# Performance work log

Measured on AMD Instinct MI355X. Metric: run time of the kernel, lower is better.

## Reference

```python
import jax, jax.numpy as jnp
import numpy as np

D_MODEL, D_STATE, D_CONV, EXPAND, N_HEADS = 768, 64, 4, 2, 12
D_INNER = D_MODEL * EXPAND           # 1536
HEAD_DIM = D_INNER // N_HEADS        # 128
IN_PROJ = D_INNER * 2 + N_HEADS * D_STATE * 2 + N_HEADS  # 4620
EPS = 1e-5


def setup_inputs() -> dict:
    key = jax.random.key(0)
    ks = jax.random.split(key, 8)
    s = lambda fan_in: 1.0 / np.sqrt(fan_in)
    return {
        "x": jax.random.normal(ks[0], (1, 1024, D_MODEL), dtype=jnp.float32),
        "W_in": jax.random.normal(ks[1], (IN_PROJ, D_MODEL), dtype=jnp.float32) * s(D_MODEL),
        "conv_w": jax.random.normal(ks[2], (D_INNER, D_CONV), dtype=jnp.float32) * s(D_CONV),
        "conv_b": jnp.zeros((D_INNER,), dtype=jnp.float32),
        "A_log": jnp.full((N_HEADS,), np.log(0.5), dtype=jnp.float32),
        "Dp": jnp.ones((N_HEADS,), dtype=jnp.float32),
        "dt_bias": jnp.zeros((N_HEADS,), dtype=jnp.float32),
        "W_out": jax.random.normal(ks[3], (D_MODEL, D_INNER), dtype=jnp.float32) * s(D_INNER),
        "norm_w": jnp.ones((D_INNER,), dtype=jnp.float32),
    }


def _causal_conv1d(x, w, b):
    # x: (B,L,Din), depthwise causal conv with kernel size D_CONV
    L = x.shape[1]
    xp = jnp.pad(x, ((0, 0), (D_CONV - 1, 0), (0, 0)))
    y = b
    for i in range(D_CONV):  # fixed small kernel, unrolled
        y = y + xp[:, i:i + L, :] * w[:, i]
    return y


def reference(x, W_in, conv_w, conv_b, A_log, Dp, dt_bias, W_out, norm_w):
    B_sz, L, _ = x.shape
    nh, ds, hd = N_HEADS, D_STATE, HEAD_DIM
    proj = jnp.einsum('bld,pd->blp', x, W_in)
    z = proj[:, :, :D_INNER]
    x_ssm = proj[:, :, D_INNER:2 * D_INNER]
    o = 2 * D_INNER
    Bm = proj[:, :, o:o + nh * ds].reshape(B_sz, L, nh, ds)
    Cm = proj[:, :, o + nh * ds:o + 2 * nh * ds].reshape(B_sz, L, nh, ds)
    dt_r = proj[:, :, o + 2 * nh * ds:]
    dt = jax.nn.softplus(dt_r) + dt_bias[None, None, :]          # (B,L,nh)

    x_ssm = jax.nn.silu(_causal_conv1d(x_ssm, conv_w, conv_b))
    x_ssm = x_ssm.reshape(B_sz, L, nh, hd)

    A = -jnp.exp(A_log)                                          # (nh,)
    log_decay = A[None, None, :] * dt                            # (B,L,nh)
    Phi = jnp.cumsum(log_decay, axis=1)
    dB = dt[..., None] * Bm                                      # (B,L,nh,ds)
    # b: (B,L,nh,hd,ds) outer product
    b = dB[:, :, :, None, :] * x_ssm[..., None]
    max_exp = 80.0
    exp_neg_Phi = jnp.exp(jnp.minimum(-Phi, max_exp))[..., None, None]
    b_cumsum = jnp.cumsum(exp_neg_Phi * b, axis=1)
    h = jnp.exp(Phi)[..., None, None] * b_cumsum                 # (B,L,nh,hd,ds)
    y = jnp.sum(Cm[:, :, :, None, :] * h, axis=-1)               # (B,L,nh,hd)
    y = y + Dp[None, None, :, None] * x_ssm
    y = y.reshape(B_sz, L, D_INNER)

    # RMSNorm then gate
    rms = jax.lax.rsqrt(jnp.mean(y * y, axis=-1, keepdims=True) + EPS)
    y = y * rms * norm_w
    y = y * jax.nn.silu(z)
    return jnp.einsum('bli,di->bld', y, W_out)
```

## Files before the change

### kernel.cpp

```cpp
#include <hip/hip_runtime.h>
#include <cmath>

#define LSEQ   1024
#define NPROJ  4620
#define NPADW  4736
#define DINNER 1536
#define NH     12
#define HDIM   128
#define OFF_Z  0
#define OFF_X  1536
#define OFF_B  3072
#define OFF_C  3840
#define OFF_DT 4608

typedef unsigned short u16;
typedef unsigned int u32;
typedef short bf16x8 __attribute__((ext_vector_type(8)));
typedef float f32x4 __attribute__((ext_vector_type(4)));

__device__ inline u16 f2b(float f) {
  unsigned u = __float_as_uint(f);
  return (u16)((u + 0x7fffu + ((u >> 16) & 1u)) >> 16);
}
__device__ inline float b2f(u16 h) { return __uint_as_float(((unsigned)h) << 16); }
__device__ inline u32 pk2(float a, float b) { return (u32)f2b(a) | ((u32)f2b(b) << 16); }

__device__ inline void gll16(const void* g, void* l) {
  __builtin_amdgcn_global_load_lds((const __attribute__((address_space(1))) void*)g,
                                   (__attribute__((address_space(3))) void*)l, 16, 0, 0);
}

#define S0N 196608
#define S1N 909312
#define S1V 887040
#define S2N 294912
__global__ __launch_bounds__(256) void ksplit_all(const float* __restrict__ x,
    const float* __restrict__ Wi, u16* __restrict__ Ah, u16* __restrict__ Wh) {
  int i = blockIdx.x * 256 + threadIdx.x;
  const float* src; u16* hi; int j, valid;
  if (i < S0N) { src = x;  hi = Ah; j = i;       valid = S0N; }
  else         { src = Wi; hi = Wh; j = i - S0N; valid = S1V; }
  float4 v = (j < valid) ? ((const float4*)src)[j] : make_float4(0.f, 0.f, 0.f, 0.f);
  ((uint2*)hi)[j] = make_uint2(pk2(v.x, v.y), pk2(v.z, v.w));
}

template<int BM, int BN, int MAP, bool NG>
__global__ __launch_bounds__(256) void gemm1(const u16* __restrict__ Ah,
    const u16* __restrict__ Wh, float* __restrict__ C,
    int lda, int ldw, int Ksl, int Nreal, int ldc) {
  constexpr int PLA = BM * 64;
  constexpr int IA = BM / 8, ITOT = IA + BN / 8;
  constexpr int FRn = BN / 32;
  __shared__ u16 lds[PLA + BN * 64];
  const int tid = threadIdx.x;
  const int l = tid & 63, w = tid >> 6;
  const int wm = w >> 1, wn = w & 1;
  const int kg = l >> 4, li = l & 15;

  int b = blockIdx.x, m0, n0, koff;
  float* Cp = C;
  if (MAP == 0) {
    int xcd = b & 7, idx = b >> 3;
    m0 = (idx & 15) * 64;
    n0 = (xcd * 5 + (idx >> 4)) * 128;
    koff = 0;
    if (NG && n0 >= NPADW) return;
  } else {
    int xcd = b & 7, idx = b >> 3;
    int gg = xcd * 6 + (idx >> 4);
    m0 = (idx & 15) * 64;
    n0 = (gg % 12) * 64;
    koff = (gg / 12) * 384;
    Cp = C + (size_t)(gg / 12) * LSEQ * ldc;
  }

  const int srcg = ((l & 7) ^ (l >> 3)) * 8;
  auto stage = [&](int t) {
    const int k0 = koff + t * 64;
    for (int q = w; q < ITOT; q += 4) {
      const u16* gb; int r0b, ldk, dst;
      if (q < IA) { gb = Ah; r0b = m0 + 8 * q;        dst = 8 * q * 64;              ldk = lda; }
      else        { gb = Wh; r0b = n0 + 8 * (q - IA); dst = PLA + 8 * (q - IA) * 64; ldk = ldw; }
      gll16(gb + (size_t)(r0b + (l >> 3)) * ldk + k0 + srcg, &lds[dst]);
    }
  };
  auto rd = [&](int region, int row, int ks) -> bf16x8 {
    return *(const bf16x8*)&lds[region + row * 64 + (((ks * 4 + kg) ^ (row & 7)) << 3)];
  };

  f32x4 acc[2][FRn];
#pragma unroll
  for (int m = 0; m < 2; ++m)
#pragma unroll
    for (int n = 0; n < FRn; ++n) acc[m][n] = (f32x4){0.f, 0.f, 0.f, 0.f};

  const int NT = Ksl / 64;
  stage(0);
  asm volatile("s_waitcnt vmcnt(0)" ::: "memory");
  __syncthreads();
  for (int t = 0; t < NT; ++t) {
    bf16x8 af[2][2], wf[FRn][2];
#pragma unroll
    for (int ks = 0; ks < 2; ++ks) {
#pragma unroll
      for (int m = 0; m < 2; ++m)
        af[m][ks] = rd(0, wm * 32 + m * 16 + li, ks);
#pragma unroll
      for (int n = 0; n < FRn; ++n)
        wf[n][ks] = rd(PLA, wn * (BN / 2) + n * 16 + li, ks);
    }
    __syncthreads();
    if (t + 1 < NT) stage(t + 1);
#pragma unroll
    for (int ks = 0; ks < 2; ++ks)
#pragma unroll
      for (int m = 0; m < 2; ++m)
#pragma unroll
        for (int n = 0; n < FRn; ++n)
          acc[m][n] = __builtin_amdgcn_mfma_f32_16x16x32_bf16(af[m][ks], wf[n][ks], acc[m][n], 0, 0, 0);
    if (t + 1 < NT) {
      asm volatile("s_waitcnt vmcnt(0)" ::: "memory");
      __syncthreads();
    }
  }
#pragma unroll
  for (int m = 0; m < 2; ++m) {
    int rbase = m0 + wm * 32 + m * 16 + kg * 4;
#pragma unroll
    for (int n = 0; n < FRn; ++n) {
      int col = n0 + wn * (BN / 2) + n * 16 + li;
      if (!NG || col < Nreal) {
#pragma unroll
        for (int r = 0; r < 4; ++r)
          Cp[(size_t)(rbase + r) * ldc + col] = acc[m][n][r];
      }
    }
  }
}

__global__ __launch_bounds__(256) void addk(const float* __restrict__ P,
    const float* __restrict__ rmsacc, float* __restrict__ out) {
  const int S = LSEQ * 768 / 4;
  int i = blockIdx.x * 256 + threadIdx.x;
  int t = i / 192;
  float rms = rsqrtf(rmsacc[t] * (1.f / 1536.f) + 1e-5f);
  float4 a = ((const float4*)P)[i];
  float4 b = ((const float4*)P)[i + S];
  float4 c = ((const float4*)P)[i + 2 * S];
  float4 d = ((const float4*)P)[i + 3 * S];
  ((float4*)out)[i] = make_float4((a.x + b.x + c.x + d.x) * rms,
                                  (a.y + b.y + c.y + d.y) * rms,
                                  (a.z + b.z + c.z + d.z) * rms,
                                  (a.w + b.w + c.w + d.w) * rms);
}

__global__ __launch_bounds__(256) void conv_state(const float* __restrict__ proj,
    const float* __restrict__ cw, const float* __restrict__ cb,
    const float* __restrict__ A_log, const float* __restrict__ dt_bias,
    u16* __restrict__ xactT, float* __restrict__ SlocF,
    float* __restrict__ Phi, float* __restrict__ dts, float* __restrict__ rmsacc) {
  const int k = blockIdx.x, h = blockIdx.y, tid = threadIdx.x;
  const int l = tid & 63, w = tid >> 6, kg = l >> 4, li = l & 15;
  __shared__ u16 Bw[4096];
  __shared__ u16 Xt[8192];
  __shared__ float wS[64];
  __shared__ float wsum[4];
  __shared__ float phiC[64], dtC[64];
  const int s0 = k * 64;

  if (h == 0 && tid < 64) rmsacc[k * 64 + tid] = 0.f;
  {
    float Ac = -expf(A_log[h]);
    float bb = dt_bias[h];
    float v[4], s = 0.f;
#pragma unroll
    for (int u = 0; u < 4; ++u) {
      int t = tid * 4 + u;
      float xr = proj[(size_t)t * NPROJ + OFF_DT + h];
      float sp = (xr > 20.f) ? xr : log1pf(expf(xr));
      v[u] = sp + bb;
      s += v[u];
    }
    int lane = tid & 63, wv = tid >> 6;
    float ps = s;
#pragma unroll
    for (int d = 1; d < 64; d <<= 1) {
      float o = __shfl_up(ps, d);
      if (lane >= d) ps += o;
    }
    if (lane == 63) wsum[wv] = ps;
    __syncthreads();
    float off = 0.f;
    for (int q = 0; q < wv; ++q) off += wsum[q];
    float run = off + ps - s;
#pragma unroll
    for (int u = 0; u < 4; ++u) {
      int t = tid * 4 + u;
      run += v[u];
      if ((t >> 6) == k) {
        float ph = Ac * run;
        phiC[t & 63] = ph;
        dtC[t & 63] = v[u];
        Phi[t * NH + h] = ph;
        dts[t * NH + h] = v[u];
      }
    }
  }
  __syncthreads();
  if (tid < 64) wS[tid] = expf(phiC[63] + fminf(-phiC[tid], 80.f)) * dtC[tid];
  __syncthreads();
#pragma unroll
  for (int u = 0; u < 4; ++u) {
    int idx = tid + u * 256, s = idx >> 4, q = (idx & 15) * 4;
    float4 v = *(const float4*)(proj + (size_t)(s0 + s) * NPROJ + OFF_B + h * 64 + q);
    float ws_ = wS[s];
    float vv[4] = {v.x, v.y, v.z, v.w};
#pragma unroll
    for (int j = 0; j < 4; ++j) {
      int d = q + j;
      Bw[d * 64 + (((s >> 3) ^ (d & 7)) << 3) + (s & 7)] = f2b(vv[j] * ws_);
    }
  }
  {
    int c = tid & 127, th = tid >> 7;
    int cg = h * HDIM + c;
    float w0 = cw[cg * 4], w1 = cw[cg * 4 + 1], w2 = cw[cg * 4 + 2], w3 = cw[cg * 4 + 3];
    float bias = cb[cg];
    int tb = s0 + th * 32;
    auto P = [&](int t) { return (t >= 0) ? proj[(size_t)t * NPROJ + OFF_X + cg] : 0.f; };
    float x0 = P(tb - 3), x1 = P(tb - 2), x2 = P(tb - 1);
    u32 pkb[16];
    float prev = 0.f;
#pragma unroll
    for (int i = 0; i < 32; ++i) {
      float x3 = P(tb + i);
      float a = bias;
      a = fmaf(x0, w0, a); a = fmaf(x1, w1, a); a = fmaf(x2, w2, a); a = fmaf(x3, w3, a);
      float sv = a / (1.f + expf(-a));
      if (i & 1) pkb[i >> 1] = pk2(prev, sv); else prev = sv;
      x0 = x1; x1 = x2; x2 = x3;
    }
#pragma unroll
    for (int g = 0; g < 4; ++g) {
      int sg = th * 4 + g;
      *(uint4*)&Xt[c * 64 + ((sg ^ (c & 7)) << 3)] =
          make_uint4(pkb[g * 4], pkb[g * 4 + 1], pkb[g * 4 + 2], pkb[g * 4 + 3]);
    }
    size_t xo = ((size_t)(k * NH + h) * 128 + c) * 64 + th * 32;
#pragma unroll
    for (int g = 0; g < 4; ++g)
      *(uint4*)(xactT + xo + g * 8) =
          make_uint4(pkb[g * 4], pkb[g * 4 + 1], pkb[g * 4 + 2], pkb[g * 4 + 3]);
  }
  __syncthreads();
  const int wm = w >> 1, wn = w & 1;
  auto rd = [&](const u16* reg, int row, int ks) -> bf16x8 {
    return *(const bf16x8*)&reg[row * 64 + (((ks * 4 + kg) ^ (row & 7)) << 3)];
  };
  f32x4 acc[4][2];
#pragma unroll
  for (int m = 0; m < 4; ++m)
#pragma unroll
    for (int n = 0; n < 2; ++n) acc[m][n] = (f32x4){0.f, 0.f, 0.f, 0.f};
#pragma unroll
  for (int ks = 0; ks < 2; ++ks) {
    bf16x8 xf[4], bf[2];
#pragma unroll
    for (int m = 0; m < 4; ++m) xf[m] = rd(Xt, wm * 64 + m * 16 + li, ks);
#pragma unroll
    for (int n = 0; n < 2; ++n) bf[n] = rd(Bw, wn * 32 + n * 16 + li, ks);
#pragma unroll
    for (int m = 0; m < 4; ++m)
#pragma unroll
      for (int n = 0; n < 2; ++n)
        acc[m][n] = __builtin_amdgcn_mfma_f32_16x16x32_bf16(xf[m], bf[n], acc[m][n], 0, 0, 0);
  }
  float* dst = SlocF + (((size_t)(k * NH + h)) << 13);
#pragma unroll
  for (int m = 0; m < 4; ++m)
#pragma unroll
    for (int n = 0; n < 2; ++n)
#pragma unroll
      for (int r = 0; r < 4; ++r) {
        int c = wm * 64 + m * 16 + kg * 4 + r;
        int d = wn * 32 + n * 16 + li;
        dst[c * 64 + d] = acc[m][n][r];
      }
}

__global__ __launch_bounds__(256) void chunk_scan(const float* __restrict__ SlocF,
    u16* __restrict__ SlocT, const float* __restrict__ Phi,
    const float* __restrict__ Wo, u16* __restrict__ Woh) {
  int gi = blockIdx.x * 256 + threadIdx.x;
#pragma unroll
  for (int it = 0; it < 3; ++it) {
    int j = gi + it * 98304;
    float4 vv = ((const float4*)Wo)[j];
    ((uint2*)Woh)[j] = make_uint2(pk2(vv.x, vv.y), pk2(vv.z, vv.w));
  }
  int b = blockIdx.x;
  int h = b >> 5;
  int e = (b & 31) * 256 + threadIdx.x;
  float run = SlocF[((size_t)h << 13) + e];
  SlocT[((size_t)h << 13) + e] = f2b(run);
#pragma unroll
  for (int k = 1; k < 16; ++k) {
    float lam = expf(Phi[(k * 64 + 63) * NH + h] - Phi[(k * 64 - 1) * NH + h]);
    size_t o = ((size_t)(k * NH + h) << 13) + e;
    run = fmaf(lam, run, SlocF[o]);
    SlocT[o] = f2b(run);
  }
}

__global__ __launch_bounds__(256) void ssm_out(const float* __restrict__ proj,
    const u16* __restrict__ xactT, const float* __restrict__ Phi,
    const float* __restrict__ dts, const float* __restrict__ Dp,
    const u16* __restrict__ SlocT, const float* __restrict__ nw,
    u16* __restrict__ Yh, float* __restrict__ rmsacc) {
  const int k = blockIdx.x, h = blockIdx.y, zh = blockIdx.z, tid = threadIdx.x;
  const int l = tid & 63, w = tid >> 6, kg = l >> 4, li = l & 15;
  const int wm = w >> 1, wn = w & 1;
  __shared__ u16 Cs[4096], Bs[4096], Ps[4096], Xs[4096], Ss[4096];
  __shared__ float phiT[64], eSs[64], dSs[64], eTs[64];
  __shared__ float sq[64], nws[64];
  const int t0 = k * 64;
  const int srcg = ((l & 7) ^ (l >> 3)) * 8;
  {
#pragma unroll
    for (int j = 0; j < 2; ++j) {
      int rb = w * 16 + j * 8;
      gll16(xactT + ((size_t)(k * NH + h) * 128 + zh * 64 + rb + (l >> 3)) * 64 + srcg, &Xs[rb * 64]);
    }
    if (k > 0) {
      const u16* ssrc = SlocT + (((size_t)((k - 1) * NH + h) * 128 + zh * 64)) * 64;
#pragma unroll
      for (int j = 0; j < 2; ++j) {
        int rb = w * 16 + j * 8;
        gll16(ssrc + (size_t)(rb + (l >> 3)) * 64 + srcg, &Ss[rb * 64]);
      }
    }
  }
#pragma unroll
  for (int u = 0; u < 4; ++u) {
    int idx = tid + u * 256, i = idx >> 4, q = (idx & 15) * 4;
    int aoff = i * 64 + (((q >> 3) ^ (i & 7)) << 3) + (q & 4);
    float4 cv = *(const float4*)(proj + (size_t)(t0 + i) * NPROJ + OFF_C + h * 64 + q);
    float4 bv = *(const float4*)(proj + (size_t)(t0 + i) * NPROJ + OFF_B + h * 64 + q);
    *(uint2*)&Cs[aoff] = make_uint2(pk2(cv.x, cv.y), pk2(cv.z, cv.w));
    *(uint2*)&Bs[aoff] = make_uint2(pk2(bv.x, bv.y), pk2(bv.z, bv.w));
  }
  if (tid < 64) {
    float p = Phi[(t0 + tid) * NH + h];
    phiT[tid] = p;
    eSs[tid] = fminf(-p, 80.f);
    dSs[tid] = dts[(t0 + tid) * NH + h];
    eTs[tid] = (k > 0) ? expf(p - Phi[(t0 - 1) * NH + h]) : 0.f;
    sq[tid] = 0.f;
    nws[tid] = nw[h * HDIM + zh * 64 + tid];
  }
  __syncthreads();
  auto rd = [&](const u16* reg, int row, int ks) -> bf16x8 {
    return *(const bf16x8*)&reg[row * 64 + (((ks * 4 + kg) ^ (row & 7)) << 3)];
  };
  bf16x8 Cf[2][2];
  f32x4 accS[2][2];
#pragma unroll
  for (int m = 0; m < 2; ++m)
#pragma unroll
    for (int n = 0; n < 2; ++n) accS[m][n] = (f32x4){0.f, 0.f, 0.f, 0.f};
#pragma unroll
  for (int ks = 0; ks < 2; ++ks) {
    bf16x8 Bf[2];
#pragma unroll
    for (int m = 0; m < 2; ++m) Cf[m][ks] = rd(Cs, wm * 32 + m * 16 + li, ks);
#pragma unroll
    for (int n = 0; n < 2; ++n) Bf[n] = rd(Bs, wn * 32 + n * 16 + li, ks);
#pragma unroll
    for (int m = 0; m < 2; ++m)
#pragma unroll
      for (int n = 0; n < 2; ++n)
        accS[m][n] = __builtin_amdgcn_mfma_f32_16x16x32_bf16(Cf[m][ks], Bf[n], accS[m][n], 0, 0, 0);
  }
#pragma unroll
  for (int m = 0; m < 2; ++m)
#pragma unroll
    for (int n = 0; n < 2; ++n)
#pragma unroll
      for (int r = 0; r < 4; ++r) {
        int t = wm * 32 + m * 16 + kg * 4 + r;
        int s = wn * 32 + n * 16 + li;
        float f = (s <= t) ? expf(phiT[t] + eSs[s]) * dSs[s] : 0.f;
        Ps[t * 64 + (((s >> 3) ^ (t & 7)) << 3) + (s & 7)] = f2b(accS[m][n][r] * f);
      }
  __syncthreads();
  f32x4 accY[2][2], acc2[2][2];
#pragma unroll
  for (int m = 0; m < 2; ++m)
#pragma unroll
    for (int n = 0; n < 2; ++n) {
      accY[m][n] = (f32x4){0.f, 0.f, 0.f, 0.f};
      acc2[m][n] = (f32x4){0.f, 0.f, 0.f, 0.f};
    }
#pragma unroll
  for (int ks = 0; ks < 2; ++ks) {
    bf16x8 Pf[2], Xf[2];
#pragma unroll
    for (int m = 0; m < 2; ++m) Pf[m] = rd(Ps, wm * 32 + m * 16 + li, ks);
#pragma unroll
    for (int n = 0; n < 2; ++n) Xf[n] = rd(Xs, wn * 32 + n * 16 + li, ks);
#pragma unroll
    for (int m = 0; m < 2; ++m)
#pragma unroll
      for (int n = 0; n < 2; ++n)
        accY[m][n] = __builtin_amdgcn_mfma_f32_16x16x32_bf16(Pf[m], Xf[n], accY[m][n], 0, 0, 0);
    if (k > 0) {
      bf16x8 Sf[2];
#pragma unroll
      for (int n = 0; n < 2; ++n) Sf[n] = rd(Ss, wn * 32 + n * 16 + li, ks);
#pragma unroll
      for (int m = 0; m < 2; ++m)
#pragma unroll
        for (int n = 0; n < 2; ++n)
          acc2[m][n] = __builtin_amdgcn_mfma_f32_16x16x32_bf16(Cf[m][ks], Sf[n], acc2[m][n], 0, 0, 0);
    }
  }
  float dp = Dp[h];
  float ls[8] = {};
#pragma unroll
  for (int m = 0; m < 2; ++m)
#pragma unroll
    for (int n = 0; n < 2; ++n)
#pragma unroll
      for (int r = 0; r < 4; ++r) {
        int t = wm * 32 + m * 16 + kg * 4 + r;
        int c = wn * 32 + n * 16 + li;
        float xv = b2f(Xs[c * 64 + (((t >> 3) ^ (c & 7)) << 3) + (t & 7)]);
        float val = accY[m][n][r] + eTs[t] * acc2[m][n][r] + dp * xv;
        ls[m * 4 + r] = fmaf(val, val, ls[m * 4 + r]);
        float z = proj[(size_t)(t0 + t) * NPROJ + OFF_Z + h * HDIM + zh * 64 + c];
        float sz = z / (1.f + expf(-z));
        Yh[(size_t)(t0 + t) * DINNER + h * HDIM + zh * 64 + c] = f2b(val * nws[c] * sz);
      }
#pragma unroll
  for (int j = 0; j < 8; ++j) {
    float v = ls[j];
    v += __shfl_xor(v, 1); v += __shfl_xor(v, 2);
    v += __shfl_xor(v, 4); v += __shfl_xor(v, 8);
    if (li == 0) atomicAdd(&sq[wm * 32 + (j >> 2) * 16 + kg * 4 + (j & 3)], v);
  }
  __syncthreads();
  if (tid < 64) atomicAdd(&rmsacc[t0 + tid], sq[tid]);
}

extern "C" void kernel_launch(void* const* d_in, const int* in_sizes, int n_in,
                              void* d_out, int out_size, void* d_ws, size_t ws_size,
                              hipStream_t stream) {
  const float* x       = (const float*)d_in[0];
  const float* W_in    = (const float*)d_in[1];
  const float* conv_w  = (const float*)d_in[2];
  const float* conv_b  = (const float*)d_in[3];
  const float* A_log   = (const float*)d_in[4];
  const float* Dp      = (const float*)d_in[5];
  const float* dt_bias = (const float*)d_in[6];
  const float* W_out   = (const float*)d_in[7];
  const float* norm_w  = (const float*)d_in[8];
  float* out = (float*)d_out;

  char* base = (char*)d_ws;
  size_t o = 0;
  auto alloc = [&](size_t bytes) { char* r = base + o; o += (bytes + 255) & ~(size_t)255; return r; };
  float* proj   = (float*)alloc((size_t)LSEQ * NPROJ * 4);
  float* Phi    = (float*)alloc((size_t)LSEQ * NH * 4);
  float* dts    = (float*)alloc((size_t)LSEQ * NH * 4);
  float* rmsacc = (float*)alloc((size_t)LSEQ * 4);
  float* SlocF  = (float*)alloc((size_t)16 * NH * 8192 * 4);
  u16*   SlocT  = (u16*)alloc((size_t)16 * NH * 8192 * 2);
  u16*   xactT  = (u16*)alloc((size_t)16 * NH * 8192 * 2);
  u16*   Ah     = (u16*)alloc((size_t)LSEQ * 768 * 2);
  u16*   Wh     = (u16*)alloc((size_t)NPADW * 768 * 2);
  u16*   Woh    = (u16*)alloc((size_t)768 * DINNER * 2);
  u16*   Yh     = (u16*)alloc((size_t)LSEQ * DINNER * 2);
  float* Pp     = (float*)alloc((size_t)4 * LSEQ * 768 * 4);

  ksplit_all<<<dim3((S0N + S1N) / 256), 256, 0, stream>>>(x, W_in, Ah, Wh);
  gemm1<64, 128, 0, true><<<dim3(640), 256, 0, stream>>>(
      Ah, Wh, proj, 768, 768, 768, NPROJ, NPROJ);
  conv_state<<<dim3(16, NH), 256, 0, stream>>>(
      proj, conv_w, conv_b, A_log, dt_bias, xactT, SlocF, Phi, dts, rmsacc);
  chunk_scan<<<dim3(NH * 32), 256, 0, stream>>>(SlocF, SlocT, Phi, W_out, Woh);
  ssm_out<<<dim3(16, NH, 2), 256, 0, stream>>>(
      proj, xactT, Phi, dts, Dp, SlocT, norm_w, Yh, rmsacc);
  gemm1<64, 64, 1, false><<<dim3(768), 256, 0, stream>>>(
      Yh, Woh, Pp, 1536, 1536, 384, 768, 768);
  addk<<<dim3(LSEQ * 768 / 4 / 256), 256, 0, stream>>>(Pp, rmsacc, out);
}
```

Measured before the change: 66.83 us.

## Double K-step per GEMM iteration and store chunk states in bf16 in place

```diff
diff --git a/kernel.cpp b/kernel.cpp
--- a/kernel.cpp
+++ b/kernel.cpp
@@ -48,10 +48,10 @@
 __global__ __launch_bounds__(256) void gemm1(const u16* __restrict__ Ah,
     const u16* __restrict__ Wh, float* __restrict__ C,
     int lda, int ldw, int Ksl, int Nreal, int ldc) {
-  constexpr int PLA = BM * 64;
-  constexpr int IA = BM / 8, ITOT = IA + BN / 8;
+  constexpr int HALF = (BM + BN) * 64;
+  constexpr int IA = BM / 8, IH = IA + BN / 8;
   constexpr int FRn = BN / 32;
-  __shared__ u16 lds[PLA + BN * 64];
+  __shared__ u16 lds[2 * HALF];
   const int tid = threadIdx.x;
   const int l = tid & 63, w = tid >> 6;
   const int wm = w >> 1, wn = w & 1;
@@ -76,16 +76,18 @@
 
   const int srcg = ((l & 7) ^ (l >> 3)) * 8;
   auto stage = [&](int t) {
-    const int k0 = koff + t * 64;
-    for (int q = w; q < ITOT; q += 4) {
-      const u16* gb; int r0b, ldk, dst;
-      if (q < IA) { gb = Ah; r0b = m0 + 8 * q;        dst = 8 * q * 64;              ldk = lda; }
-      else        { gb = Wh; r0b = n0 + 8 * (q - IA); dst = PLA + 8 * (q - IA) * 64; ldk = ldw; }
-      gll16(gb + (size_t)(r0b + (l >> 3)) * ldk + k0 + srcg, &lds[dst]);
-    }
+    const int k0 = koff + t * 128;
+#pragma unroll
+    for (int kk = 0; kk < 2; ++kk)
+      for (int q = w; q < IH; q += 4) {
+        const u16* gb; int r0b, ldk, dst;
+        if (q < IA) { gb = Ah; r0b = m0 + 8 * q;        dst = kk * HALF + 8 * q * 64;              ldk = lda; }
+        else        { gb = Wh; r0b = n0 + 8 * (q - IA); dst = kk * HALF + BM * 64 + 8 * (q - IA) * 64; ldk = ldw; }
+        gll16(gb + (size_t)(r0b + (l >> 3)) * ldk + k0 + kk * 64 + srcg, &lds[dst]);
+      }
   };
-  auto rd = [&](int region, int row, int ks) -> bf16x8 {
-    return *(const bf16x8*)&lds[region + row * 64 + (((ks * 4 + kg) ^ (row & 7)) << 3)];
+  auto rd = [&](int kk, int region, int row, int ks) -> bf16x8 {
+    return *(const bf16x8*)&lds[kk * HALF + region + row * 64 + (((ks * 4 + kg) ^ (row & 7)) << 3)];
   };
 
   f32x4 acc[2][FRn];
@@ -94,21 +96,32 @@
 #pragma unroll
     for (int n = 0; n < FRn; ++n) acc[m][n] = (f32x4){0.f, 0.f, 0.f, 0.f};
 
-  const int NT = Ksl / 64;
+  const int NT = Ksl / 128;
   stage(0);
   asm volatile("s_waitcnt vmcnt(0)" ::: "memory");
   __syncthreads();
   for (int t = 0; t < NT; ++t) {
-    bf16x8 af[2][2], wf[FRn][2];
+    bf16x8 a0[2][2], w0[FRn][2], a1[2][2], w1[FRn][2];
 #pragma unroll
     for (int ks = 0; ks < 2; ++ks) {
 #pragma unroll
+      for (int m = 0; m < 2; ++m) {
+        a0[m][ks] = rd(0, 0, wm * 32 + m * 16 + li, ks);
+        a1[m][ks] = rd(1, 0, wm * 32 + m * 16 + li, ks);
+      }
+#pragma unroll
+      for (int n = 0; n < FRn; ++n) {
+        w0[n][ks] = rd(0, BM * 64, wn * (BN / 2) + n * 16 + li, ks);
+        w1[n][ks] = rd(1, BM * 64, wn * (BN / 2) + n * 16 + li, ks);
+      }
+    }
+#pragma unroll
+    for (int ks = 0; ks < 2; ++ks)
+#pragma unroll
       for (int m = 0; m < 2; ++m)
-        af[m][ks] = rd(0, wm * 32 + m * 16 + li, ks);
-#pragma unroll
-      for (int n = 0; n < FRn; ++n)
-        wf[n][ks] = rd(PLA, wn * (BN / 2) + n * 16 + li, ks);
-    }
+#pragma unroll
+        for (int n = 0; n < FRn; ++n)
+          acc[m][n] = __builtin_amdgcn_mfma_f32_16x16x32_bf16(a0[m][ks], w0[n][ks], acc[m][n], 0, 0, 0);
     __syncthreads();
     if (t + 1 < NT) stage(t + 1);
 #pragma unroll
@@ -117,7 +130,7 @@
       for (int m = 0; m < 2; ++m)
 #pragma unroll
         for (int n = 0; n < FRn; ++n)
-          acc[m][n] = __builtin_amdgcn_mfma_f32_16x16x32_bf16(af[m][ks], wf[n][ks], acc[m][n], 0, 0, 0);
+          acc[m][n] = __builtin_amdgcn_mfma_f32_16x16x32_bf16(a1[m][ks], w1[n][ks], acc[m][n], 0, 0, 0);
     if (t + 1 < NT) {
       asm volatile("s_waitcnt vmcnt(0)" ::: "memory");
       __syncthreads();
@@ -157,7 +170,7 @@
 __global__ __launch_bounds__(256) void conv_state(const float* __restrict__ proj,
     const float* __restrict__ cw, const float* __restrict__ cb,
     const float* __restrict__ A_log, const float* __restrict__ dt_bias,
-    u16* __restrict__ xactT, float* __restrict__ SlocF,
+    u16* __restrict__ xactT, u16* __restrict__ Sloc,
     float* __restrict__ Phi, float* __restrict__ dts, float* __restrict__ rmsacc) {
   const int k = blockIdx.x, h = blockIdx.y, tid = threadIdx.x;
   const int l = tid & 63, w = tid >> 6, kg = l >> 4, li = l & 15;
@@ -275,7 +288,7 @@
       for (int n = 0; n < 2; ++n)
         acc[m][n] = __builtin_amdgcn_mfma_f32_16x16x32_bf16(xf[m], bf[n], acc[m][n], 0, 0, 0);
   }
-  float* dst = SlocF + (((size_t)(k * NH + h)) << 13);
+  u16* dst = Sloc + (((size_t)(k * NH + h)) << 13);
 #pragma unroll
   for (int m = 0; m < 4; ++m)
 #pragma unroll
@@ -284,13 +297,12 @@
       for (int r = 0; r < 4; ++r) {
         int c = wm * 64 + m * 16 + kg * 4 + r;
         int d = wn * 32 + n * 16 + li;
-        dst[c * 64 + d] = acc[m][n][r];
-      }
-}
-
-__global__ __launch_bounds__(256) void chunk_scan(const float* __restrict__ SlocF,
-    u16* __restrict__ SlocT, const float* __restrict__ Phi,
-    const float* __restrict__ Wo, u16* __restrict__ Woh) {
+        dst[c * 64 + d] = f2b(acc[m][n][r]);
+      }
+}
+
+__global__ __launch_bounds__(256) void chunk_scan(u16* __restrict__ Sloc,
+    const float* __restrict__ Phi, const float* __restrict__ Wo, u16* __restrict__ Woh) {
   int gi = blockIdx.x * 256 + threadIdx.x;
 #pragma unroll
   for (int it = 0; it < 3; ++it) {
@@ -301,21 +313,20 @@
   int b = blockIdx.x;
   int h = b >> 5;
   int e = (b & 31) * 256 + threadIdx.x;
-  float run = SlocF[((size_t)h << 13) + e];
-  SlocT[((size_t)h << 13) + e] = f2b(run);
+  float run = b2f(Sloc[((size_t)h << 13) + e]);
 #pragma unroll
   for (int k = 1; k < 16; ++k) {
     float lam = expf(Phi[(k * 64 + 63) * NH + h] - Phi[(k * 64 - 1) * NH + h]);
     size_t o = ((size_t)(k * NH + h) << 13) + e;
-    run = fmaf(lam, run, SlocF[o]);
-    SlocT[o] = f2b(run);
+    run = fmaf(lam, run, b2f(Sloc[o]));
+    Sloc[o] = f2b(run);
   }
 }
 
 __global__ __launch_bounds__(256) void ssm_out(const float* __restrict__ proj,
     const u16* __restrict__ xactT, const float* __restrict__ Phi,
     const float* __restrict__ dts, const float* __restrict__ Dp,
-    const u16* __restrict__ SlocT, const float* __restrict__ nw,
+    const u16* __restrict__ Sloc, const float* __restrict__ nw,
     u16* __restrict__ Yh, float* __restrict__ rmsacc) {
   const int k = blockIdx.x, h = blockIdx.y, zh = blockIdx.z, tid = threadIdx.x;
   const int l = tid & 63, w = tid >> 6, kg = l >> 4, li = l & 15;
@@ -332,7 +343,7 @@
       gll16(xactT + ((size_t)(k * NH + h) * 128 + zh * 64 + rb + (l >> 3)) * 64 + srcg, &Xs[rb * 64]);
     }
     if (k > 0) {
-      const u16* ssrc = SlocT + (((size_t)((k - 1) * NH + h) * 128 + zh * 64)) * 64;
+      const u16* ssrc = Sloc + (((size_t)((k - 1) * NH + h) * 128 + zh * 64)) * 64;
 #pragma unroll
       for (int j = 0; j < 2; ++j) {
         int rb = w * 16 + j * 8;
@@ -473,8 +484,7 @@
   float* Phi    = (float*)alloc((size_t)LSEQ * NH * 4);
   float* dts    = (float*)alloc((size_t)LSEQ * NH * 4);
   float* rmsacc = (float*)alloc((size_t)LSEQ * 4);
-  float* SlocF  = (float*)alloc((size_t)16 * NH * 8192 * 4);
-  u16*   SlocT  = (u16*)alloc((size_t)16 * NH * 8192 * 2);
+  u16*   Sloc   = (u16*)alloc((size_t)16 * NH * 8192 * 2);
   u16*   xactT  = (u16*)alloc((size_t)16 * NH * 8192 * 2);
   u16*   Ah     = (u16*)alloc((size_t)LSEQ * 768 * 2);
   u16*   Wh     = (u16*)alloc((size_t)NPADW * 768 * 2);
@@ -486,10 +496,10 @@
   gemm1<64, 128, 0, true><<<dim3(640), 256, 0, stream>>>(
       Ah, Wh, proj, 768, 768, 768, NPROJ, NPROJ);
   conv_state<<<dim3(16, NH), 256, 0, stream>>>(
-      proj, conv_w, conv_b, A_log, dt_bias, xactT, SlocF, Phi, dts, rmsacc);
-  chunk_scan<<<dim3(NH * 32), 256, 0, stream>>>(SlocF, SlocT, Phi, W_out, Woh);
+      proj, conv_w, conv_b, A_log, dt_bias, xactT, Sloc, Phi, dts, rmsacc);
+  chunk_scan<<<dim3(NH * 32), 256, 0, stream>>>(Sloc, Phi, W_out, Woh);
   ssm_out<<<dim3(16, NH, 2), 256, 0, stream>>>(
-      proj, xactT, Phi, dts, Dp, SlocT, norm_w, Yh, rmsacc);
+      proj, xactT, Phi, dts, Dp, Sloc, norm_w, Yh, rmsacc);
   gemm1<64, 64, 1, false><<<dim3(768), 256, 0, stream>>>(
       Yh, Woh, Pp, 1536, 1536, 384, 768, 768);
   addk<<<dim3(LSEQ * 768 / 4 / 256), 256, 0, stream>>>(Pp, rmsacc, out);
```

Result: no change. 66.42 us, median of 2 (-0.6%).
